# Performance work log

Measured on AMD Instinct MI355X. Metric: run time of the kernel, lower is better.

## Reference

```python
import jax, jax.numpy as jnp
import numpy as np

N = 20000   # nodes
E = 320000  # edges
NE = 2000   # entities
H = 4       # attention heads
D = 128     # hidden_dim (per-head out feats)
K = 10      # knn k


def _gat(h, src, dst, W, al, ar, Wr, relu):
    # h: [N, Fin]; W: [H*D, Fin]; al/ar: [H, D]; Wr: [H*D, Fin]
    feat = (h @ W.T).reshape(N, H, D)                      # [N,H,D]
    el = jnp.sum(feat * al[None], axis=-1)                 # [N,H]
    er = jnp.sum(feat * ar[None], axis=-1)                 # [N,H]
    e = jax.nn.leaky_relu(el[src] + er[dst], 0.2)          # [E,H]
    emax = jax.ops.segment_max(e, dst, num_segments=N)
    emax = jnp.where(jnp.isfinite(emax), emax, 0.0)
    a = jnp.exp(e - emax[dst])                             # [E,H]
    asum = jax.ops.segment_sum(a, dst, num_segments=N)
    asum = jnp.where(asum > 0, asum, 1.0)
    alpha = a / asum[dst]                                  # edge softmax over incoming edges
    msg = alpha[:, :, None] * feat[src]                    # [E,H,D]
    rst = jax.ops.segment_sum(msg, dst, num_segments=N)    # [N,H,D]
    rst = rst + (h @ Wr.T).reshape(N, H, D)                # residual
    if relu:
        rst = jax.nn.relu(rst)
    return rst


def _mlp2(x, W1, b1, W2, b2):
    return jax.nn.sigmoid(jax.nn.relu(x @ W1.T + b1) @ W2.T + b2)


def setup_inputs() -> dict:
    key = jax.random.key(0)
    ks = jax.random.split(key, 32)
    f32 = jnp.float32
    p = lambda i, s: (jax.random.normal(ks[i], s, dtype=f32) * 0.05)
    inp = {
        'position': jax.random.normal(ks[0], (N, 2), dtype=f32),
        'w_embed': jax.random.normal(ks[1], (N, 126), dtype=f32),
        'src': jax.random.randint(ks[2], (E,), 0, N),
        'dst': jax.random.randint(ks[3], (E,), 0, N),
        'entity': jax.random.randint(ks[4], (N,), 0, NE),
        # GAT layer 1 (in=128)
        'W1': p(5, (H * D, 128)), 'al1': p(6, (H, D)), 'ar1': p(7, (H, D)), 'Wr1': p(8, (H * D, 128)),
        # GAT layer 2 (in=512)
        'W2': p(9, (H * D, H * D)), 'al2': p(10, (H, D)), 'ar2': p(11, (H, D)), 'Wr2': p(12, (H * D, H * D)),
        # GAT layer 3 (in=512)
        'W3': p(13, (H * D, H * D)), 'al3': p(14, (H, D)), 'ar3': p(15, (H, D)), 'Wr3': p(16, (H * D, H * D)),
        # w_group_mlp
        'Wg1': p(17, (D, D)), 'bg1': p(18, (D,)), 'Wg2': p(19, (1, D)), 'bg2': p(20, (1,)),
        # entity_linear
        'We': p(21, (D, D)), 'be': p(22, (D,)),
        # entity_link_mlp
        'Wl1': p(23, (D, D)), 'bl1': p(24, (D,)), 'Wl2': p(25, (1, D)), 'bl2': p(26, (1,)),
        # entity_classify
        'Wc': p(27, (4, D)), 'bc': p(28, (4,)),
    }
    return inp


def reference(position, w_embed, src, dst, entity,
              W1, al1, ar1, Wr1, W2, al2, ar2, Wr2, W3, al3, ar3, Wr3,
              Wg1, bg1, Wg2, bg2, We, be, Wl1, bl1, Wl2, bl2, Wc, bc):
    h = jnp.concatenate([position, w_embed], axis=1)        # [N,128]
    h = _gat(h, src, dst, W1, al1, ar1, Wr1, True).reshape(N, H * D)
    h = _gat(h, src, dst, W2, al2, ar2, Wr2, True).reshape(N, H * D)
    h = _gat(h, src, dst, W3, al3, ar3, Wr3, False).mean(axis=1)  # [N,D]

    # pairwise group score over edges
    groups_score = _mlp2(jnp.abs(h[src] - h[dst]), Wg1, bg1, Wg2, bg2).squeeze(-1)  # [E]

    # per-entity segment reduce
    ent_sum = jax.ops.segment_sum(h, entity, num_segments=NE)            # [NE,D]
    entity_states = ent_sum @ We.T + be                                  # [NE,D]
    pos_sum = jax.ops.segment_sum(position, entity, num_segments=NE)     # [NE,2]
    cnt = jax.ops.segment_sum(jnp.ones((N,), jnp.float32), entity, num_segments=NE)
    entity_positions = pos_sum / jnp.maximum(cnt, 1.0)[:, None]          # [NE,2]

    # knn graph on entity centroids (k=10, includes self like dgl.knn_graph)
    d2 = jnp.sum((entity_positions[:, None, :] - entity_positions[None, :, :]) ** 2, axis=-1)  # [NE,NE]
    _, knn_idx = jax.lax.top_k(-d2, K)                                   # [NE,K]
    src_e = knn_idx.reshape(-1)                                          # [NE*K]
    dst_e = jnp.repeat(jnp.arange(NE), K)
    entity_link_score = _mlp2(jnp.abs(entity_states[src_e] - entity_states[dst_e]),
                              Wl1, bl1, Wl2, bl2).squeeze(-1)            # [NE*K]

    entity_class = jax.nn.sigmoid(entity_states @ Wc.T + bc)             # [NE,4]
    return (groups_score, entity_class, entity_positions, entity_link_score)
```

## Files before the change

### kernel.cpp

```cpp
#include <hip/hip_runtime.h>
#include <math.h>

#define N_NODES 20000
#define N_EDGES 320000
#define NENT    2000
#define KNN_K   10

typedef __attribute__((ext_vector_type(4))) float f32x4;
typedef __attribute__((ext_vector_type(8))) short bf16x8;
typedef __attribute__((ext_vector_type(8))) unsigned short u16x8;
typedef __attribute__((ext_vector_type(4))) unsigned short u16x4;

__device__ __forceinline__ unsigned short f2bf(float f) {
  union { float f; unsigned u; } v; v.f = f;
  unsigned r = v.u + 0x7fffu + ((v.u >> 16) & 1u);
  return (unsigned short)(r >> 16);
}
__device__ __forceinline__ float bf2f(unsigned short u) {
  union { unsigned u; float f; } v; v.u = ((unsigned)u) << 16;
  return v.f;
}
__device__ __forceinline__ float sigmoidf(float x) {
  return 1.f / (1.f + __expf(-x));
}
__device__ __forceinline__ void gload_lds16(const unsigned short* g, unsigned short* lds) {
  __builtin_amdgcn_global_load_lds(
      (const __attribute__((address_space(1))) unsigned int*)g,
      (__attribute__((address_space(3))) unsigned int*)lds, 16, 0, 0);
}

__global__ void k_build_h0(const float* __restrict__ pos, const float* __restrict__ wemb,
                           unsigned short* __restrict__ h0) {
  int i = blockIdx.x * blockDim.x + threadIdx.x;
  if (i >= N_NODES * 128) return;
  int n = i >> 7, c = i & 127;
  float v = (c < 2) ? pos[n * 2 + c] : wemb[n * 126 + (c - 2)];
  h0[i] = f2bf(v);
}

__global__ void k_f2bf(const float* __restrict__ in, unsigned short* __restrict__ out, int n) {
  int i = blockIdx.x * blockDim.x + threadIdx.x;
  if (i * 4 >= n) return;
  f32x4 v = *(const f32x4*)(in + i * 4);
  u16x4 o;
  o[0] = f2bf(v[0]); o[1] = f2bf(v[1]); o[2] = f2bf(v[2]); o[3] = f2bf(v[3]);
  *(u16x4*)(out + i * 4) = o;
}

__global__ void k_conv_weights(
    const float* __restrict__ W1, const float* __restrict__ Wr1,
    const float* __restrict__ W2, const float* __restrict__ Wr2,
    const float* __restrict__ W3, const float* __restrict__ Wr3,
    const float* __restrict__ Wg1, const float* __restrict__ Wl1,
    unsigned short* __restrict__ wbf1, unsigned short* __restrict__ wbf2,
    unsigned short* __restrict__ wbf3, unsigned short* __restrict__ wg1b,
    unsigned short* __restrict__ wl1b) {
  int i4 = (blockIdx.x * blockDim.x + threadIdx.x) * 4;
  const float* src;
  unsigned short* dst;
  if (i4 < 131072) {
    src = (i4 < 65536) ? (W1 + i4) : (Wr1 + i4 - 65536);
    dst = wbf1 + i4;
  } else if ((i4 -= 131072) < 524288) {
    src = (i4 < 262144) ? (W2 + i4) : (Wr2 + i4 - 262144);
    dst = wbf2 + i4;
  } else if ((i4 -= 524288) < 524288) {
    src = (i4 < 262144) ? (W3 + i4) : (Wr3 + i4 - 262144);
    dst = wbf3 + i4;
  } else if ((i4 -= 524288) < 32768) {
    const float* W = (i4 < 16384) ? Wg1 : Wl1;
    unsigned short* O = (i4 < 16384) ? wg1b : wl1b;
    int ii = i4 & 16383;
    int row = ii >> 7, k = ii & 127;
    int sg = (k >> 3) ^ (row & 15);
    src = W + ii;
    dst = O + row * 128 + sg * 8 + (k & 7);
  } else {
    return;
  }
  f32x4 v = *(const f32x4*)src;
  u16x4 o;
  o[0] = f2bf(v[0]); o[1] = f2bf(v[1]); o[2] = f2bf(v[2]); o[3] = f2bf(v[3]);
  *(u16x4*)dst = o;
}

__global__ __launch_bounds__(256) void k_gemm_bt(
    const unsigned short* __restrict__ A, const unsigned short* __restrict__ B,
    unsigned short* __restrict__ C, int M, int Nc, int K, int nbm) {
  const int id = blockIdx.x;
  const int bm128 = (id & 7) + 8 * (id >> 6);
  const int bn128 = (id >> 3) & 7;
  if (bm128 >= nbm) return;
  __shared__ __align__(16) unsigned short As[128 * 64];
  __shared__ __align__(16) unsigned short Bs[128 * 64];
  const int bm = bm128 * 128, bn = bn128 * 128;
  const int t = threadIdx.x;
  const int l = t & 63, w = t >> 6;
  const int wr = w >> 1, wc = w & 1;
  f32x4 acc[4][4];
#pragma unroll
  for (int m = 0; m < 4; ++m)
#pragma unroll
    for (int n = 0; n < 4; ++n) acc[m][n] = (f32x4){0.f, 0.f, 0.f, 0.f};

  for (int kb = 0; kb < K; kb += 64) {
    __syncthreads();
#pragma unroll
    for (int i = 0; i < 4; ++i) {
      int c = t + 256 * i;
      int row = c >> 3, cc = c & 7;
      int scc = cc ^ (row & 7);
      int ar = bm + row; if (ar > M - 1) ar = M - 1;
      gload_lds16(A + (size_t)ar * K + kb + scc * 8, &As[(size_t)(w * 64 + 256 * i) * 8]);
      gload_lds16(B + (size_t)(bn + row) * K + kb + scc * 8,
                  &Bs[(size_t)(w * 64 + 256 * i) * 8]);
    }
    __syncthreads();
#pragma unroll
    for (int kk = 0; kk < 2; ++kk) {
      bf16x8 af[4], bfr[4];
#pragma unroll
      for (int m = 0; m < 4; ++m) {
        int row = wr * 64 + m * 16 + (l & 15);
        int g = (kk * 4 + (l >> 4)) ^ (row & 7);
        af[m] = *(const bf16x8*)&As[row * 64 + g * 8];
      }
#pragma unroll
      for (int n = 0; n < 4; ++n) {
        int row = wc * 64 + n * 16 + (l & 15);
        int g = (kk * 4 + (l >> 4)) ^ (row & 7);
        bfr[n] = *(const bf16x8*)&Bs[row * 64 + g * 8];
      }
#pragma unroll
      for (int m = 0; m < 4; ++m)
#pragma unroll
        for (int n = 0; n < 4; ++n)
          acc[m][n] = __builtin_amdgcn_mfma_f32_16x16x32_bf16(af[m], bfr[n], acc[m][n], 0, 0, 0);
    }
  }
#pragma unroll
  for (int m = 0; m < 4; ++m) {
    int r0 = bm + wr * 64 + m * 16 + ((l >> 4) << 2);
#pragma unroll
    for (int n = 0; n < 4; ++n) {
      int c0 = bn + wc * 64 + n * 16 + (l & 15);
#pragma unroll
      for (int r = 0; r < 4; ++r) {
        int row = r0 + r;
        if (row < M) C[(size_t)row * Nc + c0] = f2bf(acc[m][n][r]);
      }
    }
  }
}

__global__ void k_el_er(const unsigned short* __restrict__ feat, int fstride,
                        const float* __restrict__ al, const float* __restrict__ ar,
                        float* __restrict__ el, float* __restrict__ er) {
  int wid = (blockIdx.x * blockDim.x + threadIdx.x) >> 6;
  if (wid >= N_NODES) return;
  int l = threadIdx.x & 63;
  int g = l >> 4, q = l & 15;
  u16x8 fv = *(const u16x8*)(feat + (size_t)wid * fstride + l * 8);
  const float* alp = al + g * 128 + q * 8;
  const float* arp = ar + g * 128 + q * 8;
  float sl = 0.f, sr = 0.f;
#pragma unroll
  for (int j = 0; j < 8; ++j) { float f = bf2f(fv[j]); sl += f * alp[j]; sr += f * arp[j]; }
#pragma unroll
  for (int d = 1; d < 16; d <<= 1) { sl += __shfl_xor(sl, d); sr += __shfl_xor(sr, d); }
  if (q == 0) { el[wid * 4 + g] = sl; er[wid * 4 + g] = sr; }
}

__global__ void k_hist(const int* __restrict__ dst, int* __restrict__ indeg) {
  int e = blockIdx.x * blockDim.x + threadIdx.x;
  if (e < N_EDGES) atomicAdd(&indeg[dst[e]], 1);
}

__global__ __launch_bounds__(1024) void k_scan_fast(const int* __restrict__ indeg,
                                                    int* __restrict__ indptr,
                                                    int* __restrict__ cursor) {
  __shared__ int wsum[16];
  const int t = threadIdx.x;
  const int l = t & 63, w = t >> 6;
  const int CH = 20;
  int base = t * CH;
  int vals[CH];
  int s = 0;
#pragma unroll
  for (int i = 0; i < CH; ++i) {
    int idx = base + i;
    int v = (idx < N_NODES) ? indeg[idx] : 0;
    vals[i] = v;
    s += v;
  }
  int ss = s;
#pragma unroll
  for (int d = 1; d < 64; d <<= 1) { int o = __shfl_up(ss, d); if (l >= d) ss += o; }
  if (l == 63) wsum[w] = ss;
  __syncthreads();
  if (t < 16) {
    int v = wsum[t];
#pragma unroll
    for (int d = 1; d < 16; d <<= 1) { int o = __shfl_up(v, d); if (t >= d) v += o; }
    wsum[t] = v;
  }
  __syncthreads();
  int run = ((w > 0) ? wsum[w - 1] : 0) + ss - s;
  if (t == 0) indptr[0] = 0;
#pragma unroll
  for (int i = 0; i < CH; ++i) {
    int idx = base + i;
    if (idx < N_NODES) {
      cursor[idx] = run;
      run += vals[i];
      indptr[idx + 1] = run;
    }
  }
}

__global__ void k_scatter(const int* __restrict__ src, const int* __restrict__ dst,
                          int* __restrict__ cursor, int* __restrict__ csr_src) {
  int e = blockIdx.x * blockDim.x + threadIdx.x;
  if (e < N_EDGES) {
    int p = atomicAdd(&cursor[dst[e]], 1);
    csr_src[p] = src[e];
  }
}

template <bool FINAL>
__global__ void k_gat_agg(const unsigned short* __restrict__ feat,
                          const unsigned short* __restrict__ hres, int fstride,
                          const float* __restrict__ el, const float* __restrict__ er,
                          const int* __restrict__ indptr, const int* __restrict__ csr_src,
                          unsigned short* __restrict__ hnext, float* __restrict__ h3,
                          unsigned short* __restrict__ h3b) {
  int wid = (blockIdx.x * blockDim.x + threadIdx.x) >> 6;
  if (wid >= N_NODES) return;
  int l = threadIdx.x & 63;
  int g = l >> 4;
  int beg = indptr[wid], end = indptr[wid + 1];
  float er_g = er[wid * 4 + g];
  float asum = 0.f;
  float acc[8];
#pragma unroll
  for (int j2 = 0; j2 < 8; ++j2) acc[j2] = 0.f;
  const unsigned short* fbase = feat + l * 8;
  int j = beg;
  for (; j + 4 <= end; j += 4) {
    int s0 = csr_src[j + 0], s1 = csr_src[j + 1];
    int s2 = csr_src[j + 2], s3 = csr_src[j + 3];
    float q0 = el[s0 * 4 + g], q1 = el[s1 * 4 + g];
    float q2 = el[s2 * 4 + g], q3 = el[s3 * 4 + g];
    u16x8 f0 = *(const u16x8*)(fbase + (size_t)s0 * fstride);
    u16x8 f1 = *(const u16x8*)(fbase + (size_t)s1 * fstride);
    u16x8 f2 = *(const u16x8*)(fbase + (size_t)s2 * fstride);
    u16x8 f3 = *(const u16x8*)(fbase + (size_t)s3 * fstride);
    float e0 = q0 + er_g; e0 = (e0 >= 0.f) ? e0 : 0.2f * e0;
    float e1 = q1 + er_g; e1 = (e1 >= 0.f) ? e1 : 0.2f * e1;
    float e2 = q2 + er_g; e2 = (e2 >= 0.f) ? e2 : 0.2f * e2;
    float e3 = q3 + er_g; e3 = (e3 >= 0.f) ? e3 : 0.2f * e3;
    float p0 = __expf(e0), p1 = __expf(e1);
    float p2 = __expf(e2), p3 = __expf(e3);
    asum += (p0 + p1) + (p2 + p3);
#pragma unroll
    for (int k = 0; k < 8; ++k)
      acc[k] += p0 * bf2f(f0[k]) + p1 * bf2f(f1[k]) + p2 * bf2f(f2[k]) + p3 * bf2f(f3[k]);
  }
  for (; j < end; ++j) {
    int s = csr_src[j];
    float ev = el[s * 4 + g] + er_g;
    ev = (ev >= 0.f) ? ev : 0.2f * ev;
    float p = __expf(ev);
    asum += p;
    u16x8 fv = *(const u16x8*)(fbase + (size_t)s * fstride);
#pragma unroll
    for (int k = 0; k < 8; ++k) acc[k] += p * bf2f(fv[k]);
  }
  float inv = (end > beg) ? 1.f / asum : 1.f;
  u16x8 hv = *(const u16x8*)(hres + (size_t)wid * fstride + l * 8);
  float o[8];
#pragma unroll
  for (int k = 0; k < 8; ++k) o[k] = acc[k] * inv + bf2f(hv[k]);
  if constexpr (!FINAL) {
    u16x8 ob;
#pragma unroll
    for (int k = 0; k < 8; ++k) ob[k] = f2bf(fmaxf(o[k], 0.f));
    *(u16x8*)(hnext + (size_t)wid * 512 + l * 8) = ob;
  } else {
#pragma unroll
    for (int k = 0; k < 8; ++k) {
      float v = o[k];
      v += __shfl_xor(v, 16);
      v += __shfl_xor(v, 32);
      o[k] = v * 0.25f;
    }
    if (g == 0) {
      f32x4 o0 = (f32x4){o[0], o[1], o[2], o[3]};
      f32x4 o1 = (f32x4){o[4], o[5], o[6], o[7]};
      *(f32x4*)(h3 + (size_t)wid * 128 + l * 8) = o0;
      *(f32x4*)(h3 + (size_t)wid * 128 + l * 8 + 4) = o1;
      u16x8 hb;
#pragma unroll
      for (int k = 0; k < 8; ++k) hb[k] = f2bf(o[k]);
      *(u16x8*)(h3b + (size_t)wid * 128 + l * 8) = hb;
    }
  }
}

template <int MODE>
__global__ __launch_bounds__(256) void k_pair_mlp(
    const unsigned short* __restrict__ X, const int* __restrict__ ia,
    const int* __restrict__ ib, const unsigned short* __restrict__ WbSwz,
    const float* __restrict__ b1, const float* __restrict__ W2,
    const float* __restrict__ b2, float* __restrict__ out, int npairs) {
  __shared__ __align__(16) unsigned short Ws[128 * 128];
  const int t = threadIdx.x;
  const int l = t & 63, w = t >> 6;
#pragma unroll
  for (int i = 0; i < 8; ++i)
    gload_lds16(WbSwz + i * 2048 + w * 512 + l * 8, &Ws[i * 2048 + w * 512]);
  const int base = blockIdx.x * 128 + w * 32;
  bf16x8 af[2][4];
#pragma unroll
  for (int m = 0; m < 2; ++m) {
    int e = base + m * 16 + (l & 15);
    if (MODE == 1 && e >= npairs) e = npairs - 1;
    int sa, sb;
    if (MODE == 0) { sa = ia[e]; sb = ib[e]; }
    else           { sa = ia[e]; sb = e / KNN_K; }
    const unsigned short* pa = X + (size_t)sa * 128 + (l >> 4) * 8;
    const unsigned short* pb = X + (size_t)sb * 128 + (l >> 4) * 8;
#pragma unroll
    for (int kk = 0; kk < 4; ++kk) {
      u16x8 av = *(const u16x8*)(pa + kk * 32);
      u16x8 bv = *(const u16x8*)(pb + kk * 32);
      u16x8 xv;
#pragma unroll
      for (int j = 0; j < 8; ++j) xv[j] = f2bf(fabsf(bf2f(av[j]) - bf2f(bv[j])));
      af[m][kk] = *(bf16x8*)&xv;
    }
  }
  __syncthreads();
  float part[2][4];
#pragma unroll
  for (int m = 0; m < 2; ++m)
#pragma unroll
    for (int r = 0; r < 4; ++r) part[m][r] = 0.f;
#pragma unroll
  for (int n = 0; n < 8; ++n) {
    int rowv = n * 16 + (l & 15);
    bf16x8 bfr[4];
#pragma unroll
    for (int kk = 0; kk < 4; ++kk) {
      int sg = (kk * 4 + (l >> 4)) ^ (rowv & 15);
      bfr[kk] = *(const bf16x8*)&Ws[rowv * 128 + sg * 8];
    }
    f32x4 acc0 = (f32x4){0.f, 0.f, 0.f, 0.f};
    f32x4 acc1 = (f32x4){0.f, 0.f, 0.f, 0.f};
#pragma unroll
    for (int kk = 0; kk < 4; ++kk) {
      acc0 = __builtin_amdgcn_mfma_f32_16x16x32_bf16(af[0][kk], bfr[kk], acc0, 0, 0, 0);
      acc1 = __builtin_amdgcn_mfma_f32_16x16x32_bf16(af[1][kk], bfr[kk], acc1, 0, 0, 0);
    }
    float bb = b1[rowv], w2v = W2[rowv];
#pragma unroll
    for (int r = 0; r < 4; ++r) {
      part[0][r] += fmaxf(acc0[r] + bb, 0.f) * w2v;
      part[1][r] += fmaxf(acc1[r] + bb, 0.f) * w2v;
    }
  }
#pragma unroll
  for (int d = 1; d < 16; d <<= 1)
#pragma unroll
    for (int m = 0; m < 2; ++m)
#pragma unroll
      for (int r = 0; r < 4; ++r) part[m][r] += __shfl_xor(part[m][r], d);
  if ((l & 15) == 0) {
    int q = l >> 4;
    float b2v = b2[0];
#pragma unroll
    for (int m = 0; m < 2; ++m) {
      int e = base + m * 16 + q * 4;
      f32x4 ov;
#pragma unroll
      for (int r = 0; r < 4; ++r) ov[r] = sigmoidf(part[m][r] + b2v);
      if (e + 3 < npairs) *(f32x4*)(out + e) = ov;
      else {
#pragma unroll
        for (int r = 0; r < 4; ++r) if (e + r < npairs) out[e + r] = ov[r];
      }
    }
  }
}

__global__ void k_ent_scatter(const float* __restrict__ h3, const float* __restrict__ pos,
                              const int* __restrict__ entity, float* __restrict__ ent_sum,
                              float* __restrict__ pos_sum, float* __restrict__ cnt) {
  int i = blockIdx.x * blockDim.x + threadIdx.x;
  if (i >= N_NODES * 32) return;
  int n = i >> 5, c = i & 31;
  int e = entity[n];
  f32x4 v = *(const f32x4*)(h3 + (size_t)n * 128 + c * 4);
  atomicAdd(&ent_sum[e * 128 + c * 4 + 0], v[0]);
  atomicAdd(&ent_sum[e * 128 + c * 4 + 1], v[1]);
  atomicAdd(&ent_sum[e * 128 + c * 4 + 2], v[2]);
  atomicAdd(&ent_sum[e * 128 + c * 4 + 3], v[3]);
  if (c == 0) {
    atomicAdd(&pos_sum[e * 2 + 0], pos[n * 2 + 0]);
    atomicAdd(&pos_sum[e * 2 + 1], pos[n * 2 + 1]);
    atomicAdd(&cnt[e], 1.f);
  }
}

__global__ void k_entity_states(const float* __restrict__ ent_sum, const float* __restrict__ We,
                                const float* __restrict__ be, float* __restrict__ es) {
  int i = blockIdx.x * blockDim.x + threadIdx.x;
  if (i >= NENT * 128) return;
  int e = i >> 7, j = i & 127;
  const float* x = ent_sum + (size_t)e * 128;
  const float* wrow = We + (size_t)j * 128;
  float s = be[j];
  for (int k = 0; k < 128; k += 4) {
    f32x4 xv = *(const f32x4*)(x + k);
    f32x4 wv = *(const f32x4*)(wrow + k);
    s += xv[0] * wv[0] + xv[1] * wv[1] + xv[2] * wv[2] + xv[3] * wv[3];
  }
  es[i] = s;
}

__global__ void k_entity_class(const float* __restrict__ es, const float* __restrict__ Wc,
                               const float* __restrict__ bc, float* __restrict__ out) {
  int i = blockIdx.x * blockDim.x + threadIdx.x;
  if (i >= NENT * 4) return;
  int e = i >> 2, c = i & 3;
  const float* x = es + (size_t)e * 128;
  const float* wrow = Wc + (size_t)c * 128;
  float s = bc[c];
  for (int k = 0; k < 128; ++k) s += x[k] * wrow[k];
  out[i] = sigmoidf(s);
}

__global__ void k_entity_pos(const float* __restrict__ pos_sum, const float* __restrict__ cnt,
                             float* __restrict__ outpos, float* __restrict__ wspos) {
  int e = blockIdx.x * blockDim.x + threadIdx.x;
  if (e >= NENT) return;
  float c = fmaxf(cnt[e], 1.f);
  float x = pos_sum[e * 2] / c, y = pos_sum[e * 2 + 1] / c;
  outpos[e * 2] = x; outpos[e * 2 + 1] = y;
  wspos[e * 2] = x; wspos[e * 2 + 1] = y;
}

__global__ __launch_bounds__(256) void k_knn(const float* __restrict__ entpos,
                                             int* __restrict__ knn) {
  __shared__ float d2row[NENT];
  __shared__ float rv[256];
  __shared__ int ri[256];
  int i = blockIdx.x, t = threadIdx.x;
  float px = entpos[i * 2], py = entpos[i * 2 + 1];
  for (int j = t; j < NENT; j += 256) {
    float dx = px - entpos[j * 2], dy = py - entpos[j * 2 + 1];
    d2row[j] = __fadd_rn(__fmul_rn(dx, dx), __fmul_rn(dy, dy));
  }
  __syncthreads();
  for (int k = 0; k < KNN_K; ++k) {
    float bv = __builtin_inff(); int bi = 0x7fffffff;
    for (int j = t; j < NENT; j += 256) {
      float v = d2row[j];
      if (v < bv) { bv = v; bi = j; }
    }
    rv[t] = bv; ri[t] = bi;
    __syncthreads();
    for (int s = 128; s > 0; s >>= 1) {
      if (t < s) {
        if (rv[t + s] < rv[t] || (rv[t + s] == rv[t] && ri[t + s] < ri[t])) {
          rv[t] = rv[t + s]; ri[t] = ri[t + s];
        }
      }
      __syncthreads();
    }
    if (t == 0) { knn[i * KNN_K + k] = ri[0]; d2row[ri[0]] = __builtin_inff(); }
    __syncthreads();
  }
}

extern "C" void kernel_launch(void* const* d_in, const int* in_sizes, int n_in,
                              void* d_out, int out_size, void* d_ws, size_t ws_size,
                              hipStream_t stream) {
  const float* position = (const float*)d_in[0];
  const float* w_embed  = (const float*)d_in[1];
  const int*   src      = (const int*)d_in[2];
  const int*   dst      = (const int*)d_in[3];
  const int*   entity   = (const int*)d_in[4];
  const float* W1 = (const float*)d_in[5];
  const float* al1 = (const float*)d_in[6];
  const float* ar1 = (const float*)d_in[7];
  const float* Wr1 = (const float*)d_in[8];
  const float* W2 = (const float*)d_in[9];
  const float* al2 = (const float*)d_in[10];
  const float* ar2 = (const float*)d_in[11];
  const float* Wr2 = (const float*)d_in[12];
  const float* W3 = (const float*)d_in[13];
  const float* al3 = (const float*)d_in[14];
  const float* ar3 = (const float*)d_in[15];
  const float* Wr3 = (const float*)d_in[16];
  const float* Wg1 = (const float*)d_in[17];
  const float* bg1 = (const float*)d_in[18];
  const float* Wg2 = (const float*)d_in[19];
  const float* bg2 = (const float*)d_in[20];
  const float* We  = (const float*)d_in[21];
  const float* be  = (const float*)d_in[22];
  const float* Wl1 = (const float*)d_in[23];
  const float* bl1 = (const float*)d_in[24];
  const float* Wl2 = (const float*)d_in[25];
  const float* bl2 = (const float*)d_in[26];
  const float* Wc  = (const float*)d_in[27];
  const float* bc  = (const float*)d_in[28];

  float* out_groups = (float*)d_out;
  float* out_class  = out_groups + N_EDGES;
  float* out_pos    = out_class + NENT * 4;
  float* out_link   = out_pos + NENT * 2;

  char* ws = (char*)d_ws;
  size_t off = 0;
  auto carve = [&](size_t bytes) -> char* {
    char* p = ws + off;
    off = (off + bytes + 255) & ~(size_t)255;
    return p;
  };
  unsigned short* featC = (unsigned short*)carve((size_t)N_NODES * 1024 * 2);
  unsigned short* hA = (unsigned short*)carve((size_t)N_NODES * 512 * 2);
  unsigned short* hB = (unsigned short*)carve((size_t)N_NODES * 512 * 2);
  unsigned short* wbf1 = (unsigned short*)carve((size_t)1024 * 128 * 2);
  unsigned short* wbf2 = (unsigned short*)carve((size_t)1024 * 512 * 2);
  unsigned short* wbf3 = (unsigned short*)carve((size_t)1024 * 512 * 2);
  unsigned short* wg1b = (unsigned short*)carve(128 * 128 * 2);
  unsigned short* wl1b = (unsigned short*)carve(128 * 128 * 2);
  float* el = (float*)carve((size_t)N_NODES * 4 * 4);
  float* er = (float*)carve((size_t)N_NODES * 4 * 4);
  int* indeg = (int*)carve((size_t)N_NODES * 4);
  int* indptr = (int*)carve((size_t)(N_NODES + 1) * 4);
  int* cursor = (int*)carve((size_t)N_NODES * 4);
  int* csr_src = (int*)carve((size_t)N_EDGES * 4);
  float* h3 = (float*)carve((size_t)N_NODES * 128 * 4);
  unsigned short* h3b = (unsigned short*)carve((size_t)N_NODES * 128 * 2);
  float* ent_sum = (float*)carve((size_t)NENT * 128 * 4);
  float* pos_sum = (float*)carve((size_t)NENT * 2 * 4);
  float* cnt = (float*)carve((size_t)NENT * 4);
  float* es = (float*)carve((size_t)NENT * 128 * 4);
  unsigned short* esb = (unsigned short*)carve((size_t)NENT * 128 * 2);
  float* wspos = (float*)carve((size_t)NENT * 2 * 4);
  int* knn = (int*)carve((size_t)NENT * KNN_K * 4);

  hipMemsetAsync(indeg, 0, (size_t)N_NODES * 4, stream);
  k_hist<<<(N_EDGES + 255) / 256, 256, 0, stream>>>(dst, indeg);
  k_scan_fast<<<1, 1024, 0, stream>>>(indeg, indptr, cursor);
  k_scatter<<<(N_EDGES + 255) / 256, 256, 0, stream>>>(src, dst, cursor, csr_src);

  k_build_h0<<<(N_NODES * 128 + 255) / 256, 256, 0, stream>>>(position, w_embed, hA);

  k_conv_weights<<<(303104 + 255) / 256, 256, 0, stream>>>(W1, Wr1, W2, Wr2, W3, Wr3, Wg1, Wl1,
                                                           wbf1, wbf2, wbf3, wg1b, wl1b);

  const int NBM = (N_NODES + 127) / 128;
  const int GGRID = 160 * 8;

  k_gemm_bt<<<GGRID, 256, 0, stream>>>(hA, wbf1, featC, N_NODES, 1024, 128, NBM);
  k_el_er<<<5000, 256, 0, stream>>>(featC, 1024, al1, ar1, el, er);
  k_gat_agg<false><<<5000, 256, 0, stream>>>(featC, featC + 512, 1024, el, er, indptr,
                                             csr_src, hB, nullptr, nullptr);

  k_gemm_bt<<<GGRID, 256, 0, stream>>>(hB, wbf2, featC, N_NODES, 1024, 512, NBM);
  k_el_er<<<5000, 256, 0, stream>>>(featC, 1024, al2, ar2, el, er);
  k_gat_agg<false><<<5000, 256, 0, stream>>>(featC, featC + 512, 1024, el, er, indptr,
                                             csr_src, hA, nullptr, nullptr);

  k_gemm_bt<<<GGRID, 256, 0, stream>>>(hA, wbf3, featC, N_NODES, 1024, 512, NBM);
  k_el_er<<<5000, 256, 0, stream>>>(featC, 1024, al3, ar3, el, er);
  k_gat_agg<true><<<5000, 256, 0, stream>>>(featC, featC + 512, 1024, el, er, indptr,
                                            csr_src, nullptr, h3, h3b);

  k_pair_mlp<0><<<N_EDGES / 128, 256, 0, stream>>>(h3b, src, dst, wg1b, bg1, Wg2, bg2,
                                                   out_groups, N_EDGES);

  size_t zbytes = (size_t)((char*)cnt - (char*)ent_sum) + NENT * 4;
  hipMemsetAsync(ent_sum, 0, zbytes, stream);
  k_ent_scatter<<<(N_NODES * 32 + 255) / 256, 256, 0, stream>>>(h3, position, entity, ent_sum,
                                                                pos_sum, cnt);
  k_entity_states<<<(NENT * 128 + 255) / 256, 256, 0, stream>>>(ent_sum, We, be, es);
  k_entity_class<<<(NENT * 4 + 255) / 256, 256, 0, stream>>>(es, Wc, bc, out_class);
  k_entity_pos<<<(NENT + 255) / 256, 256, 0, stream>>>(pos_sum, cnt, out_pos, wspos);
  k_knn<<<NENT, 256, 0, stream>>>(wspos, knn);
  k_f2bf<<<(NENT * 128 / 4 + 255) / 256, 256, 0, stream>>>(es, esb, NENT * 128);
  k_pair_mlp<1><<<(NENT * KNN_K + 127) / 128, 256, 0, stream>>>(esb, knn, nullptr, wl1b, bl1,
                                                                Wl2, bl2, out_link,
                                                                NENT * KNN_K);
}
```

Before: 441.0 us.

## Split GAT edge aggregation across two waves per node and fuse small kernels

The GAT aggregation now gives each destination node two wavefronts, each handling half its incoming edges, and combines the partial sums and softmax denominators through LDS. The aim is more memory-level parallelism and shorter per-wave edge loops. Separately, the h0 build and weight conversion are merged into one init kernel, and entity_states, entity_class and the bf16 conversion are fused into one per-entity kernel, removing several launches. The cost is a block-wide sync and LDS traffic in the aggregation, and half the waves exit early after the reduction.

```diff
diff --git a/kernel.cpp b/kernel.cpp
--- a/kernel.cpp
+++ b/kernel.cpp
@@ -29,33 +29,32 @@
       (__attribute__((address_space(3))) unsigned int*)lds, 16, 0, 0);
 }
 
-__global__ void k_build_h0(const float* __restrict__ pos, const float* __restrict__ wemb,
-                           unsigned short* __restrict__ h0) {
-  int i = blockIdx.x * blockDim.x + threadIdx.x;
-  if (i >= N_NODES * 128) return;
-  int n = i >> 7, c = i & 127;
-  float v = (c < 2) ? pos[n * 2 + c] : wemb[n * 126 + (c - 2)];
-  h0[i] = f2bf(v);
-}
-
-__global__ void k_f2bf(const float* __restrict__ in, unsigned short* __restrict__ out, int n) {
-  int i = blockIdx.x * blockDim.x + threadIdx.x;
-  if (i * 4 >= n) return;
-  f32x4 v = *(const f32x4*)(in + i * 4);
-  u16x4 o;
-  o[0] = f2bf(v[0]); o[1] = f2bf(v[1]); o[2] = f2bf(v[2]); o[3] = f2bf(v[3]);
-  *(u16x4*)(out + i * 4) = o;
-}
-
-__global__ void k_conv_weights(
+__global__ void k_init(
+    const float* __restrict__ pos, const float* __restrict__ wemb,
     const float* __restrict__ W1, const float* __restrict__ Wr1,
     const float* __restrict__ W2, const float* __restrict__ Wr2,
     const float* __restrict__ W3, const float* __restrict__ Wr3,
     const float* __restrict__ Wg1, const float* __restrict__ Wl1,
+    unsigned short* __restrict__ h0,
     unsigned short* __restrict__ wbf1, unsigned short* __restrict__ wbf2,
     unsigned short* __restrict__ wbf3, unsigned short* __restrict__ wg1b,
     unsigned short* __restrict__ wl1b) {
-  int i4 = (blockIdx.x * blockDim.x + threadIdx.x) * 4;
+  int tid = blockIdx.x * blockDim.x + threadIdx.x;
+  if (tid < 640000) {
+    int i = tid * 4;
+    int n = i >> 7, c = i & 127;
+    u16x4 o;
+    if (c == 0) {
+      o[0] = f2bf(pos[n * 2]); o[1] = f2bf(pos[n * 2 + 1]);
+      o[2] = f2bf(wemb[n * 126]); o[3] = f2bf(wemb[n * 126 + 1]);
+    } else {
+      const float* p = wemb + (size_t)n * 126 + (c - 2);
+      o[0] = f2bf(p[0]); o[1] = f2bf(p[1]); o[2] = f2bf(p[2]); o[3] = f2bf(p[3]);
+    }
+    *(u16x4*)(h0 + i) = o;
+    return;
+  }
+  int i4 = (tid - 640000) * 4;
   const float* src;
   unsigned short* dst;
   if (i4 < 131072) {
@@ -228,25 +227,32 @@
 }
 
 template <bool FINAL>
-__global__ void k_gat_agg(const unsigned short* __restrict__ feat,
-                          const unsigned short* __restrict__ hres, int fstride,
-                          const float* __restrict__ el, const float* __restrict__ er,
-                          const int* __restrict__ indptr, const int* __restrict__ csr_src,
-                          unsigned short* __restrict__ hnext, float* __restrict__ h3,
-                          unsigned short* __restrict__ h3b) {
-  int wid = (blockIdx.x * blockDim.x + threadIdx.x) >> 6;
-  if (wid >= N_NODES) return;
-  int l = threadIdx.x & 63;
-  int g = l >> 4;
+__global__ __launch_bounds__(256) void k_gat_agg(
+    const unsigned short* __restrict__ feat, const unsigned short* __restrict__ hres,
+    int fstride, const float* __restrict__ el, const float* __restrict__ er,
+    const int* __restrict__ indptr, const int* __restrict__ csr_src,
+    unsigned short* __restrict__ hnext, float* __restrict__ h3,
+    unsigned short* __restrict__ h3b) {
+  __shared__ float lacc[2][512];
+  __shared__ float lsum[2][4];
+  const int t = threadIdx.x;
+  const int l = t & 63, w = t >> 6;
+  const int nib = w >> 1, sub = w & 1;
+  const int wid = blockIdx.x * 2 + nib;
+  const int g = l >> 4;
   int beg = indptr[wid], end = indptr[wid + 1];
+  int cnt = end - beg;
+  int half = (cnt + 1) >> 1;
+  int jb = beg + sub * half;
+  int je = sub ? end : (beg + half);
   float er_g = er[wid * 4 + g];
   float asum = 0.f;
   float acc[8];
 #pragma unroll
-  for (int j2 = 0; j2 < 8; ++j2) acc[j2] = 0.f;
+  for (int k = 0; k < 8; ++k) acc[k] = 0.f;
   const unsigned short* fbase = feat + l * 8;
-  int j = beg;
-  for (; j + 4 <= end; j += 4) {
+  int j = jb;
+  for (; j + 4 <= je; j += 4) {
     int s0 = csr_src[j + 0], s1 = csr_src[j + 1];
     int s2 = csr_src[j + 2], s3 = csr_src[j + 3];
     float q0 = el[s0 * 4 + g], q1 = el[s1 * 4 + g];
@@ -266,7 +272,7 @@
     for (int k = 0; k < 8; ++k)
       acc[k] += p0 * bf2f(f0[k]) + p1 * bf2f(f1[k]) + p2 * bf2f(f2[k]) + p3 * bf2f(f3[k]);
   }
-  for (; j < end; ++j) {
+  for (; j < je; ++j) {
     int s = csr_src[j];
     float ev = el[s * 4 + g] + er_g;
     ev = (ev >= 0.f) ? ev : 0.2f * ev;
@@ -276,7 +282,17 @@
 #pragma unroll
     for (int k = 0; k < 8; ++k) acc[k] += p * bf2f(fv[k]);
   }
-  float inv = (end > beg) ? 1.f / asum : 1.f;
+  if (sub) {
+#pragma unroll
+    for (int k = 0; k < 8; ++k) lacc[nib][k * 64 + l] = acc[k];
+    if ((l & 15) == 0) lsum[nib][g] = asum;
+  }
+  __syncthreads();
+  if (sub) return;
+#pragma unroll
+  for (int k = 0; k < 8; ++k) acc[k] += lacc[nib][k * 64 + l];
+  asum += lsum[nib][g];
+  float inv = (cnt > 0) ? 1.f / asum : 1.f;
   u16x8 hv = *(const u16x8*)(hres + (size_t)wid * fstride + l * 8);
   float o[8];
 #pragma unroll
@@ -412,32 +428,32 @@
   }
 }
 
-__global__ void k_entity_states(const float* __restrict__ ent_sum, const float* __restrict__ We,
-                                const float* __restrict__ be, float* __restrict__ es) {
-  int i = blockIdx.x * blockDim.x + threadIdx.x;
-  if (i >= NENT * 128) return;
-  int e = i >> 7, j = i & 127;
-  const float* x = ent_sum + (size_t)e * 128;
-  const float* wrow = We + (size_t)j * 128;
-  float s = be[j];
+__global__ __launch_bounds__(128) void k_entity_fused(
+    const float* __restrict__ ent_sum, const float* __restrict__ We,
+    const float* __restrict__ be, const float* __restrict__ Wc,
+    const float* __restrict__ bc, float* __restrict__ es,
+    unsigned short* __restrict__ esb, float* __restrict__ out_class) {
+  __shared__ float xs[128];
+  __shared__ float ess[128];
+  int e = blockIdx.x, t = threadIdx.x;
+  xs[t] = ent_sum[(size_t)e * 128 + t];
+  __syncthreads();
+  const float* wrow = We + (size_t)t * 128;
+  float s = be[t];
   for (int k = 0; k < 128; k += 4) {
-    f32x4 xv = *(const f32x4*)(x + k);
     f32x4 wv = *(const f32x4*)(wrow + k);
-    s += xv[0] * wv[0] + xv[1] * wv[1] + xv[2] * wv[2] + xv[3] * wv[3];
-  }
-  es[i] = s;
-}
-
-__global__ void k_entity_class(const float* __restrict__ es, const float* __restrict__ Wc,
-                               const float* __restrict__ bc, float* __restrict__ out) {
-  int i = blockIdx.x * blockDim.x + threadIdx.x;
-  if (i >= NENT * 4) return;
-  int e = i >> 2, c = i & 3;
-  const float* x = es + (size_t)e * 128;
-  const float* wrow = Wc + (size_t)c * 128;
-  float s = bc[c];
-  for (int k = 0; k < 128; ++k) s += x[k] * wrow[k];
-  out[i] = sigmoidf(s);
+    s += xs[k] * wv[0] + xs[k + 1] * wv[1] + xs[k + 2] * wv[2] + xs[k + 3] * wv[3];
+  }
+  es[(size_t)e * 128 + t] = s;
+  esb[(size_t)e * 128 + t] = f2bf(s);
+  ess[t] = s;
+  __syncthreads();
+  if (t < 4) {
+    const float* crow = Wc + (size_t)t * 128;
+    float c = bc[t];
+    for (int k = 0; k < 128; ++k) c += ess[k] * crow[k];
+    out_class[e * 4 + t] = sigmoidf(c);
+  }
 }
 
 __global__ void k_entity_pos(const float* __restrict__ pos_sum, const float* __restrict__ cnt,
@@ -557,28 +573,27 @@
   k_scan_fast<<<1, 1024, 0, stream>>>(indeg, indptr, cursor);
   k_scatter<<<(N_EDGES + 255) / 256, 256, 0, stream>>>(src, dst, cursor, csr_src);
 
-  k_build_h0<<<(N_NODES * 128 + 255) / 256, 256, 0, stream>>>(position, w_embed, hA);
-
-  k_conv_weights<<<(303104 + 255) / 256, 256, 0, stream>>>(W1, Wr1, W2, Wr2, W3, Wr3, Wg1, Wl1,
-                                                           wbf1, wbf2, wbf3, wg1b, wl1b);
+  k_init<<<(943104 + 255) / 256, 256, 0, stream>>>(position, w_embed, W1, Wr1, W2, Wr2,
+                                                   W3, Wr3, Wg1, Wl1, hA, wbf1, wbf2, wbf3,
+                                                   wg1b, wl1b);
 
   const int NBM = (N_NODES + 127) / 128;
   const int GGRID = 160 * 8;
 
   k_gemm_bt<<<GGRID, 256, 0, stream>>>(hA, wbf1, featC, N_NODES, 1024, 128, NBM);
   k_el_er<<<5000, 256, 0, stream>>>(featC, 1024, al1, ar1, el, er);
-  k_gat_agg<false><<<5000, 256, 0, stream>>>(featC, featC + 512, 1024, el, er, indptr,
-                                             csr_src, hB, nullptr, nullptr);
+  k_gat_agg<false><<<N_NODES / 2, 256, 0, stream>>>(featC, featC + 512, 1024, el, er, indptr,
+                                                    csr_src, hB, nullptr, nullptr);
 
   k_gemm_bt<<<GGRID, 256, 0, stream>>>(hB, wbf2, featC, N_NODES, 1024, 512, NBM);
   k_el_er<<<5000, 256, 0, stream>>>(featC, 1024, al2, ar2, el, er);
-  k_gat_agg<false><<<5000, 256, 0, stream>>>(featC, featC + 512, 1024, el, er, indptr,
-                                             csr_src, hA, nullptr, nullptr);
+  k_gat_agg<false><<<N_NODES / 2, 256, 0, stream>>>(featC, featC + 512, 1024, el, er, indptr,
+                                                    csr_src, hA, nullptr, nullptr);
 
   k_gemm_bt<<<GGRID, 256, 0, stream>>>(hA, wbf3, featC, N_NODES, 1024, 512, NBM);
   k_el_er<<<5000, 256, 0, stream>>>(featC, 1024, al3, ar3, el, er);
-  k_gat_agg<true><<<5000, 256, 0, stream>>>(featC, featC + 512, 1024, el, er, indptr,
-                                            csr_src, nullptr, h3, h3b);
+  k_gat_agg<true><<<N_NODES / 2, 256, 0, stream>>>(featC, featC + 512, 1024, el, er, indptr,
+                                                   csr_src, nullptr, h3, h3b);
 
   k_pair_mlp<0><<<N_EDGES / 128, 256, 0, stream>>>(h3b, src, dst, wg1b, bg1, Wg2, bg2,
                                                    out_groups, N_EDGES);
@@ -587,11 +602,9 @@
   hipMemsetAsync(ent_sum, 0, zbytes, stream);
   k_ent_scatter<<<(N_NODES * 32 + 255) / 256, 256, 0, stream>>>(h3, position, entity, ent_sum,
                                                                 pos_sum, cnt);
-  k_entity_states<<<(NENT * 128 + 255) / 256, 256, 0, stream>>>(ent_sum, We, be, es);
-  k_entity_class<<<(NENT * 4 + 255) / 256, 256, 0, stream>>>(es, Wc, bc, out_class);
+  k_entity_fused<<<NENT, 128, 0, stream>>>(ent_sum, We, be, Wc, bc, es, esb, out_class);
   k_entity_pos<<<(NENT + 255) / 256, 256, 0, stream>>>(pos_sum, cnt, out_pos, wspos);
   k_knn<<<NENT, 256, 0, stream>>>(wspos, knn);
-  k_f2bf<<<(NENT * 128 / 4 + 255) / 256, 256, 0, stream>>>(es, esb, NENT * 128);
   k_pair_mlp<1><<<(NENT * KNN_K + 127) / 128, 256, 0, stream>>>(esb, knn, nullptr, wl1b, bl1,
                                                                 Wl2, bl2, out_link,
                                                                 NENT * KNN_K);
```

Measured after the change: 425.4 us. -3.6%, faster.
